# Performance work log

Measured on AMD Instinct MI355X. Metric: run time of the kernel, lower is better.

## Reference

```python
import jax, jax.numpy as jnp
import numpy as np

N, C = 262144, 128

def setup_inputs() -> dict:
    key = jax.random.key(0)
    k1, k2 = jax.random.split(key)
    x = jax.random.normal(k1, (N, C), dtype=jnp.float32)
    # binary label matrix (0/1 floats), as implied by the _target[i][0]==0 check
    target = jax.random.randint(k2, (N, C), 0, 2).astype(jnp.float32)
    return {"x": x, "target": target}

def reference(x, target):
    # Per-row argmax over classes (torch.max(_input[i], 0) -> idx)
    idx = jnp.argmax(x, axis=1)                      # [N]
    # Rows where idx > 0 and target[i,0] == 0 get all non-idx target entries zeroed
    cond = (idx > 0) & (target[:, 0] == 0)           # [N]
    keep = jax.nn.one_hot(idx, x.shape[1], dtype=target.dtype)  # [N, C]
    t = jnp.where(cond[:, None], target * keep, target)
    return jnp.mean(jnp.abs(x * t))
```

## Files before the change

kernel.cpp:

```cpp
#include <hip/hip_runtime.h>

#define NROWS 262144
#define NCOLS 128
#define TPB 256
#define WPB (TPB / 64)
#define NBLOCKS 4096
#define NWAVES (NBLOCKS * WPB)
#define NPAIRS (NROWS / 2)
#define U 2
#define NBATCH (NPAIRS / (NWAVES * U))

typedef float floatx4 __attribute__((ext_vector_type(4)));

__device__ __forceinline__ floatx4 ntload4(const float* p)
{
    return __builtin_nontemporal_load((const floatx4*)p);
}

__global__ __launch_bounds__(TPB) void biased_loss_partial(
    const float* __restrict__ x, const float* __restrict__ t,
    float* __restrict__ partial)
{
    const int lane = threadIdx.x & 63;
    const int waveInBlock = threadIdx.x >> 6;
    const int gw = blockIdx.x * WPB + waveInBlock;
    const int half = lane >> 5;
    const int sub  = lane & 31;

    float acc = 0.0f;

    #pragma unroll
    for (int b = 0; b < NBATCH; ++b) {
        const int pbase = (b * NWAVES + gw) * U;

        floatx4 xv[U], tv[U];
        #pragma unroll
        for (int u = 0; u < U; ++u) {
            const size_t base =
                (size_t)(2 * (pbase + u) + half) * NCOLS + (size_t)sub * 4;
            xv[u] = ntload4(x + base);
            tv[u] = ntload4(t + base);
        }

        #pragma unroll
        for (int u = 0; u < U; ++u) {
            const int c = sub * 4;
            float bv = xv[u].x; int bi = c;
            if (xv[u].y > bv) { bv = xv[u].y; bi = c + 1; }
            if (xv[u].z > bv) { bv = xv[u].z; bi = c + 2; }
            if (xv[u].w > bv) { bv = xv[u].w; bi = c + 3; }

            #pragma unroll
            for (int off = 16; off > 0; off >>= 1) {
                float ov = __shfl_xor(bv, off, 64);
                int   oi = __shfl_xor(bi, off, 64);
                if (ov > bv || (ov == bv && oi < bi)) { bv = ov; bi = oi; }
            }

            float t0 = __shfl(tv[u].x, half << 5, 64);
            const bool cond = (bi > 0) && (t0 == 0.0f);

            float c0 = fabsf(xv[u].x * tv[u].x);
            float c1 = fabsf(xv[u].y * tv[u].y);
            float c2 = fabsf(xv[u].z * tv[u].z);
            float c3 = fabsf(xv[u].w * tv[u].w);

            float s;
            if (cond) {
                s = (c     == bi ? c0 : 0.0f)
                  + (c + 1 == bi ? c1 : 0.0f)
                  + (c + 2 == bi ? c2 : 0.0f)
                  + (c + 3 == bi ? c3 : 0.0f);
            } else {
                s = (c0 + c1) + (c2 + c3);
            }
            acc += s;
        }
    }

    #pragma unroll
    for (int off = 32; off > 0; off >>= 1)
        acc += __shfl_xor(acc, off, 64);

    __shared__ float smem[WPB];
    if (lane == 0) smem[waveInBlock] = acc;
    __syncthreads();
    if (threadIdx.x == 0) {
        float bsum = 0.0f;
        #pragma unroll
        for (int w = 0; w < WPB; ++w) bsum += smem[w];
        partial[blockIdx.x] = bsum;
    }
}

__global__ __launch_bounds__(256) void reduce_partials(
    const float* __restrict__ partial, float* __restrict__ out, int n)
{
    float acc = 0.0f;
    for (int i = threadIdx.x; i < n; i += 256) acc += partial[i];
    #pragma unroll
    for (int off = 32; off > 0; off >>= 1)
        acc += __shfl_xor(acc, off, 64);
    __shared__ float smem[4];
    const int lane = threadIdx.x & 63, w = threadIdx.x >> 6;
    if (lane == 0) smem[w] = acc;
    __syncthreads();
    if (threadIdx.x == 0) {
        float s = smem[0] + smem[1] + smem[2] + smem[3];
        out[0] = s / (float)((size_t)NROWS * (size_t)NCOLS);
    }
}

extern "C" void kernel_launch(void* const* d_in, const int* in_sizes, int n_in,
                              void* d_out, int out_size, void* d_ws, size_t ws_size,
                              hipStream_t stream) {
    const float* x = (const float*)d_in[0];
    const float* t = (const float*)d_in[1];
    float* partial = (float*)d_ws;

    biased_loss_partial<<<NBLOCKS, TPB, 0, stream>>>(x, t, partial);
    reduce_partials<<<1, 256, 0, stream>>>(partial, (float*)d_out, NBLOCKS);
}
```

Before: 254.8 us.

## Assign one row per thread with a sequential argmax and no shuffles

Maps each thread to a whole 128-column row and computes a running max, the target at the max, and the full abs-product sum serially, which removes the per-row cross-lane shuffle reductions. Nontemporal loads are replaced by plain vector loads. The cost is that neighbouring lanes now read addresses 512 bytes apart, so each wave load instruction touches 64 different cache lines instead of being coalesced. The argmax-is-zero test becomes x0 != M; on ties, where the first maximum sits in column 0, this matches the reference.

```diff
diff --git a/kernel.cpp b/kernel.cpp
--- a/kernel.cpp
+++ b/kernel.cpp
@@ -4,84 +4,58 @@
 #define NCOLS 128
 #define TPB 256
 #define WPB (TPB / 64)
-#define NBLOCKS 4096
-#define NWAVES (NBLOCKS * WPB)
-#define NPAIRS (NROWS / 2)
-#define U 2
-#define NBATCH (NPAIRS / (NWAVES * U))
+#define NBLOCKS (NROWS / TPB)
 
 typedef float floatx4 __attribute__((ext_vector_type(4)));
 
-__device__ __forceinline__ floatx4 ntload4(const float* p)
-{
-    return __builtin_nontemporal_load((const floatx4*)p);
-}
-
-__global__ __launch_bounds__(TPB) void biased_loss_partial(
+__global__ __launch_bounds__(TPB) void biased_loss_rows(
     const float* __restrict__ x, const float* __restrict__ t,
     float* __restrict__ partial)
 {
-    const int lane = threadIdx.x & 63;
-    const int waveInBlock = threadIdx.x >> 6;
-    const int gw = blockIdx.x * WPB + waveInBlock;
-    const int half = lane >> 5;
-    const int sub  = lane & 31;
+    const int row = blockIdx.x * TPB + threadIdx.x;
+    const float* xr = x + (size_t)row * NCOLS;
+    const float* tr = t + (size_t)row * NCOLS;
 
-    float acc = 0.0f;
+    floatx4 xc = *(const floatx4*)xr;
+    floatx4 tc = *(const floatx4*)tr;
+    const float x0 = xc.x;
+    const float t0 = tc.x;
+
+    float M  = xc.x;
+    float tM = tc.x;
+    float S  = fabsf(xc.x * tc.x);
+
+#define STEP(v, tv)                                   \
+    do {                                              \
+        if ((v) > M) tM = (tv);      \
+        M = fmaxf(M, (v));           \
+        S += fabsf((v) * (tv));                       \
+    } while (0)
+
+    STEP(xc.y, tc.y);
+    STEP(xc.z, tc.z);
+    STEP(xc.w, tc.w);
 
     #pragma unroll
-    for (int b = 0; b < NBATCH; ++b) {
-        const int pbase = (b * NWAVES + gw) * U;
+    for (int j = 1; j < NCOLS / 4; ++j) {
+        xc = *(const floatx4*)(xr + j * 4);
+        tc = *(const floatx4*)(tr + j * 4);
+        STEP(xc.x, tc.x);
+        STEP(xc.y, tc.y);
+        STEP(xc.z, tc.z);
+        STEP(xc.w, tc.w);
+    }
+#undef STEP
 
-        floatx4 xv[U], tv[U];
-        #pragma unroll
-        for (int u = 0; u < U; ++u) {
-            const size_t base =
-                (size_t)(2 * (pbase + u) + half) * NCOLS + (size_t)sub * 4;
-            xv[u] = ntload4(x + base);
-            tv[u] = ntload4(t + base);
-        }
-
-        #pragma unroll
-        for (int u = 0; u < U; ++u) {
-            const int c = sub * 4;
-            float bv = xv[u].x; int bi = c;
-            if (xv[u].y > bv) { bv = xv[u].y; bi = c + 1; }
-            if (xv[u].z > bv) { bv = xv[u].z; bi = c + 2; }
-            if (xv[u].w > bv) { bv = xv[u].w; bi = c + 3; }
-
-            #pragma unroll
-            for (int off = 16; off > 0; off >>= 1) {
-                float ov = __shfl_xor(bv, off, 64);
-                int   oi = __shfl_xor(bi, off, 64);
-                if (ov > bv || (ov == bv && oi < bi)) { bv = ov; bi = oi; }
-            }
-
-            float t0 = __shfl(tv[u].x, half << 5, 64);
-            const bool cond = (bi > 0) && (t0 == 0.0f);
-
-            float c0 = fabsf(xv[u].x * tv[u].x);
-            float c1 = fabsf(xv[u].y * tv[u].y);
-            float c2 = fabsf(xv[u].z * tv[u].z);
-            float c3 = fabsf(xv[u].w * tv[u].w);
-
-            float s;
-            if (cond) {
-                s = (c     == bi ? c0 : 0.0f)
-                  + (c + 1 == bi ? c1 : 0.0f)
-                  + (c + 2 == bi ? c2 : 0.0f)
-                  + (c + 3 == bi ? c3 : 0.0f);
-            } else {
-                s = (c0 + c1) + (c2 + c3);
-            }
-            acc += s;
-        }
-    }
+    const bool cond = (x0 != M) && (t0 == 0.0f);
+    float acc = cond ? fabsf(M) * tM : S;
 
     #pragma unroll
     for (int off = 32; off > 0; off >>= 1)
         acc += __shfl_xor(acc, off, 64);
 
+    const int lane = threadIdx.x & 63;
+    const int waveInBlock = threadIdx.x >> 6;
     __shared__ float smem[WPB];
     if (lane == 0) smem[waveInBlock] = acc;
     __syncthreads();
@@ -118,6 +92,6 @@
     const float* t = (const float*)d_in[1];
     float* partial = (float*)d_ws;
 
-    biased_loss_partial<<<NBLOCKS, TPB, 0, stream>>>(x, t, partial);
+    biased_loss_rows<<<NBLOCKS, TPB, 0, stream>>>(x, t, partial);
     reduce_partials<<<1, 256, 0, stream>>>(partial, (float*)d_out, NBLOCKS);
 }
```

After: 281.3 us. +10.4%, slower.
